# Kernel tuning notes

Hardware: AMD Instinct MI355X
Metric: run time of the kernel (lower is better)

## Reference

```python
import jax, jax.numpy as jnp
import numpy as np

D_MODEL = 1024
N_HEADS = 16
D_K = D_MODEL // N_HEADS
B, S = 4, 2048


def setup_inputs() -> dict:
    key = jax.random.key(0)
    ks = jax.random.split(key, 9)
    sc = 1.0 / np.sqrt(D_MODEL)
    return {
        "x": jax.random.normal(ks[0], (B, S, D_MODEL), dtype=jnp.float32),
        "Wq": jax.random.normal(ks[1], (D_MODEL, D_MODEL), dtype=jnp.float32) * sc,
        "bq": jax.random.normal(ks[2], (D_MODEL,), dtype=jnp.float32) * 0.02,
        "Wk": jax.random.normal(ks[3], (D_MODEL, D_MODEL), dtype=jnp.float32) * sc,
        "bk": jax.random.normal(ks[4], (D_MODEL,), dtype=jnp.float32) * 0.02,
        "Wv": jax.random.normal(ks[5], (D_MODEL, D_MODEL), dtype=jnp.float32) * sc,
        "bv": jax.random.normal(ks[6], (D_MODEL,), dtype=jnp.float32) * 0.02,
        "Wo": jax.random.normal(ks[7], (D_MODEL, D_MODEL), dtype=jnp.float32) * sc,
        "bo": jax.random.normal(ks[8], (D_MODEL,), dtype=jnp.float32) * 0.02,
    }


def reference(x, Wq, bq, Wk, bk, Wv, bv, Wo, bo):
    b, s, _ = x.shape
    # QKV projections (torch Linear: x @ W.T + b; here weights are stored as [in, out])
    q = (x @ Wq + bq).reshape(b, s, N_HEADS, D_K).transpose(0, 2, 1, 3)  # [b,h,s,dk]
    k = (x @ Wk + bk).reshape(b, s, N_HEADS, D_K).transpose(0, 2, 1, 3)
    v = (x @ Wv + bv).reshape(b, s, N_HEADS, D_K).transpose(0, 2, 1, 3)
    scores = jnp.einsum("bhqd,bhkd->bhqk", q, k) / jnp.sqrt(jnp.float32(D_K))
    attn = jax.nn.softmax(scores, axis=-1)  # dropout=0.0 -> identity
    out = jnp.einsum("bhqk,bhkd->bhqd", attn, v)
    out = out.transpose(0, 2, 1, 3).reshape(b, s, D_MODEL)
    return out @ Wo + bo
```

## Files before the change

### kernel.cpp

```cpp
#include <hip/hip_runtime.h>
#include <hip/hip_bf16.h>

#define DM    1024
#define NH    16
#define DKH   64
#define BB    4
#define SS    2048
#define MROWS (BB*SS)
#define NQKV  (3*DM)

typedef __attribute__((ext_vector_type(8))) __bf16 bf16x8;
typedef __attribute__((ext_vector_type(4))) float f32x4;
typedef __attribute__((ext_vector_type(16))) float f32x16;
typedef __attribute__((ext_vector_type(4))) unsigned short u16x4;

__device__ __forceinline__ void gload_lds16(const void* g, void* l) {
  __builtin_amdgcn_global_load_lds((const __attribute__((address_space(1))) void*)g,
                                   (__attribute__((address_space(3))) void*)l, 16, 0, 0);
}

__device__ __forceinline__ unsigned short f2bf(float f) {
  __hip_bfloat16 h = __float2bfloat16(f);
  unsigned short u;
  __builtin_memcpy(&u, &h, 2);
  return u;
}

__device__ __forceinline__ unsigned cvtpk2(float a, float b) {
  unsigned w;
  asm("v_cvt_pk_bf16_f32 %0, %1, %2" : "=v"(w) : "v"(a), "v"(b));
  return w;
}


__global__ __launch_bounds__(256) void cvt_bf16_kernel(const float* __restrict__ in,
                                                       unsigned short* __restrict__ out, int n4) {
  int i = blockIdx.x * 256 + threadIdx.x;
  if (i >= n4) return;
  float4 v = reinterpret_cast<const float4*>(in)[i];
  u16x4 o = { f2bf(v.x), f2bf(v.y), f2bf(v.z), f2bf(v.w) };
  reinterpret_cast<u16x4*>(out)[i] = o;
}

__global__ __launch_bounds__(256) void transpose_cvt4_kernel(
    const float* __restrict__ Wq, const float* __restrict__ Wk,
    const float* __restrict__ Wv, const float* __restrict__ Wo,
    unsigned short* __restrict__ WTqkv, unsigned short* __restrict__ WTo) {
  const int z = blockIdx.z;
  const float* W = (z == 0) ? Wq : (z == 1) ? Wk : (z == 2) ? Wv : Wo;
  unsigned short* WT = (z == 3) ? WTo : (WTqkv + (long)z * DM * DM);
  __shared__ float t[32][33];
  int tx = threadIdx.x & 31, ty = threadIdx.x >> 5;
  int bx = blockIdx.x * 32, by = blockIdx.y * 32;
#pragma unroll
  for (int i = 0; i < 32; i += 8)
    t[ty + i][tx] = W[(long)(by + ty + i) * DM + bx + tx];
  __syncthreads();
#pragma unroll
  for (int i = 0; i < 32; i += 8)
    WT[(long)(bx + ty + i) * DM + by + tx] = f2bf(t[tx][ty + i]);
}

__global__ void concat3_bias_kernel(const float* __restrict__ a, const float* __restrict__ b,
                                    const float* __restrict__ c, float* __restrict__ out) {
  int i = blockIdx.x * 256 + threadIdx.x;
  if (i >= NQKV) return;
  out[i] = (i < DM) ? a[i] : (i < 2 * DM) ? b[i - DM] : c[i - 2 * DM];
}


template <int MODE>
__global__ __launch_bounds__(256) void gemm_bt_kernel(
    const unsigned short* __restrict__ A,
    const unsigned short* __restrict__ BT,
    const float* __restrict__ bias,
    void* __restrict__ out0, void* __restrict__ out1, void* __restrict__ out2,
    int M, int N, int K) {
  __shared__ __align__(16) unsigned short smem[16384];
  const int tid = threadIdx.x;
  const int lane = tid & 63;
  const int lr = lane & 15, lg = lane >> 4;
  const int wv = tid >> 6, wm = wv >> 1, wn = wv & 1;
  const long bm = blockIdx.x, bn = blockIdx.y;

  const unsigned short* Ag = A + bm * 128 * K;
  const unsigned short* Bg = BT + bn * 128 * K;

  f32x4 acc[4][4];
#pragma unroll
  for (int i = 0; i < 4; ++i)
#pragma unroll
    for (int j = 0; j < 4; ++j) acc[i][j] = (f32x4){0.f, 0.f, 0.f, 0.f};

  auto issue = [&](int buf, int kt) {
#pragma unroll
    for (int it = 0; it < 2; ++it) {
      const int e = it * 2048 + tid * 8;
      const int row = e >> 5, col = e & 31;
      gload_lds16(Ag + (long)row * K + kt * 32 + col, smem + buf * 4096 + e);
      gload_lds16(Bg + (long)row * K + kt * 32 + col, smem + 8192 + buf * 4096 + e);
    }
  };

  const int NT = K / 32;
  issue(0, 0);
  issue(1, 1);
  asm volatile("s_waitcnt vmcnt(4)" ::: "memory");
  __builtin_amdgcn_s_barrier();

  for (int t = 0; t < NT; ++t) {
    const int buf = t & 1;
    const unsigned short* As_ = smem + buf * 4096;
    const unsigned short* Bs_ = smem + 8192 + buf * 4096;

    bf16x8 af[4], bfr[4];
#pragma unroll
    for (int mi = 0; mi < 4; ++mi)
      af[mi] = *reinterpret_cast<const bf16x8*>(As_ + (wm * 64 + mi * 16 + lr) * 32 + lg * 8);
#pragma unroll
    for (int ni = 0; ni < 4; ++ni)
      bfr[ni] = *reinterpret_cast<const bf16x8*>(Bs_ + (wn * 64 + ni * 16 + lr) * 32 + lg * 8);
    __builtin_amdgcn_s_setprio(1);
#pragma unroll
    for (int mi = 0; mi < 4; ++mi)
#pragma unroll
      for (int ni = 0; ni < 4; ++ni)
        acc[mi][ni] = __builtin_amdgcn_mfma_f32_16x16x32_bf16(af[mi], bfr[ni], acc[mi][ni], 0, 0, 0);
    __builtin_amdgcn_s_setprio(0);

    if (t + 1 < NT) {
      asm volatile("s_waitcnt lgkmcnt(0)" ::: "memory");
      __builtin_amdgcn_s_barrier();
      if (t + 2 < NT) {
        issue(buf, t + 2);
        asm volatile("s_waitcnt vmcnt(4)" ::: "memory");
      } else {
        asm volatile("s_waitcnt vmcnt(0)" ::: "memory");
      }
      __builtin_amdgcn_s_barrier();
      asm volatile("" ::: "memory");
    }
  }

  const float QSC = 0.125f * 1.44269504088896340736f;
#pragma unroll
  for (int ni = 0; ni < 4; ++ni) {
    const int col = (int)bn * 128 + wn * 64 + ni * 16 + lr;
    const float bc = bias[col];
#pragma unroll
    for (int mi = 0; mi < 4; ++mi) {
      const int row0 = (int)bm * 128 + wm * 64 + mi * 16 + lg * 4;
#pragma unroll
      for (int r = 0; r < 4; ++r) {
        const int row = row0 + r;
        float v = acc[mi][ni][r] + bc;
        if (MODE == 0) {
          if (col < DM) {
            ((unsigned short*)out0)[(long)row * DM + col] = f2bf(v * QSC);
          } else if (col < 2 * DM) {
            const int c2 = col - DM;
            const int h = c2 >> 6, dh = c2 & 63;
            const int b = row >> 11, s = row & 2047;
            const long idx = ((((long)(b * NH + h) * 32 + (s >> 6)) * 512 +
                               (dh >> 3) * 64 + (s & 63)) << 3) + (dh & 7);
            ((unsigned short*)out1)[idx] = f2bf(v);
          } else {
            const int c2 = col - 2 * DM;
            const int h = c2 >> 6, dh = c2 & 63;
            const int b = row >> 11, s = row & 2047;
            const long idx = ((((long)(b * NH + h) * 32 + (s >> 6)) * 512 +
                               ((s >> 3) & 7) * 64 + dh) << 3) + (s & 7);
            ((unsigned short*)out2)[idx] = f2bf(v);
          }
        } else {
          ((float*)out0)[(long)row * (long)N + col] = v;
        }
      }
    }
  }
}


__global__ __launch_bounds__(256, 3) void attn_kernel(
    const unsigned short* __restrict__ Qb,
    const unsigned short* __restrict__ Kf,
    const unsigned short* __restrict__ Vf,
    unsigned short* __restrict__ AO) {
  __shared__ __align__(16) unsigned short sK[2][4096];
  __shared__ __align__(16) unsigned short sV[2][4096];

  const int tid = threadIdx.x;
  const int lane = tid & 63;
  const int wv = tid >> 6;
  const int q5 = lane & 31;
  const int hi = lane >> 5;

  const int bh = blockIdx.x;
  const int qt = blockIdx.y;
  const int b = bh >> 4, h = bh & 15;

  bf16x8 qf[4];
  {
    const unsigned short* qrow = Qb + (long)(b * SS + qt * 128 + wv * 32 + q5) * DM + h * DKH;
#pragma unroll
    for (int dstep = 0; dstep < 4; ++dstep)
      qf[dstep] = *reinterpret_cast<const bf16x8*>(qrow + dstep * 16 + hi * 8);
  }

  const unsigned short* Kp = Kf + (long)bh * 32 * 4096;
  const unsigned short* Vp = Vf + (long)bh * 32 * 4096;

  f32x16 accv[2];
#pragma unroll
  for (int d = 0; d < 2; ++d)
#pragma unroll
    for (int r = 0; r < 16; ++r) accv[d][r] = 0.f;
  f32x16 lacc;
#pragma unroll
  for (int r = 0; r < 16; ++r) lacc[r] = 0.f;

  f32x16 zc;
#pragma unroll
  for (int r = 0; r < 16; ++r) zc[r] = 0.f;

  auto stage = [&](int buf, int t) {
#pragma unroll
    for (int it = 0; it < 2; ++it) {
      const int u = it * 256 + tid;
      gload_lds16(Kp + (long)t * 4096 + u * 8, &sK[buf][u * 8]);
      gload_lds16(Vp + (long)t * 4096 + u * 8, &sV[buf][u * 8]);
    }
  };

  stage(0, 0);
  __syncthreads();

#pragma unroll 1
  for (int kt = 0; kt < SS / 64; ++kt) {
    const int cur = kt & 1;
    if (kt + 1 < SS / 64) stage(cur ^ 1, kt + 1);
    const unsigned short* K_ = sK[cur];
    const unsigned short* V_ = sV[cur];

    f32x16 s4[2];
    __builtin_amdgcn_s_setprio(1);
#pragma unroll
    for (int kb = 0; kb < 2; ++kb)
#pragma unroll
      for (int dstep = 0; dstep < 4; ++dstep) {
        bf16x8 kf = *reinterpret_cast<const bf16x8*>(
            K_ + ((dstep * 2 + hi) * 64 + kb * 32 + q5) * 8);
        s4[kb] = __builtin_amdgcn_mfma_f32_32x32x16_bf16(kf, qf[dstep],
                                                         dstep ? s4[kb] : zc, 0, 0, 0);
      }
    __builtin_amdgcn_s_setprio(0);

#pragma unroll
    for (int kb = 0; kb < 2; ++kb)
#pragma unroll
      for (int r = 0; r < 16; ++r)
        s4[kb][r] = __builtin_amdgcn_exp2f(s4[kb][r]);
#pragma unroll
    for (int r = 0; r < 16; ++r) lacc[r] += s4[0][r] + s4[1][r];

#pragma unroll
    for (int step = 0; step < 4; ++step) {
      const int kb = step >> 1, rb = (step & 1) * 8;
      unsigned w0, w1, w2, w3;
      asm("v_cvt_pk_bf16_f32 %0, %1, %2" : "=v"(w0) : "v"(s4[kb][rb + 0]), "v"(s4[kb][rb + 1]));
      asm("v_cvt_pk_bf16_f32 %0, %1, %2" : "=v"(w1) : "v"(s4[kb][rb + 2]), "v"(s4[kb][rb + 3]));
      asm("v_cvt_pk_bf16_f32 %0, %1, %2" : "=v"(w2) : "v"(s4[kb][rb + 4]), "v"(s4[kb][rb + 5]));
      asm("v_cvt_pk_bf16_f32 %0, %1, %2" : "=v"(w3) : "v"(s4[kb][rb + 6]), "v"(s4[kb][rb + 7]));
      asm("v_permlane32_swap_b32 %0, %1" : "+v"(w0), "+v"(w2));
      asm("v_permlane32_swap_b32 %0, %1" : "+v"(w1), "+v"(w3));
      union { unsigned u[4]; bf16x8 v; } pf;
      pf.u[0] = w0;
      pf.u[1] = w1;
      pf.u[2] = w2;
      pf.u[3] = w3;
      __builtin_amdgcn_s_setprio(1);
#pragma unroll
      for (int dblk = 0; dblk < 2; ++dblk) {
        bf16x8 vf = *reinterpret_cast<const bf16x8*>(
            V_ + ((step * 2 + hi) * 64 + dblk * 32 + q5) * 8);
        accv[dblk] = __builtin_amdgcn_mfma_f32_32x32x16_bf16(vf, pf.v, accv[dblk], 0, 0, 0);
      }
      __builtin_amdgcn_s_setprio(0);
    }
    __syncthreads();
  }

  float l01 = (lacc[0] + lacc[1]) + (lacc[2] + lacc[3]);
  float l23 = (lacc[4] + lacc[5]) + (lacc[6] + lacc[7]);
  float l45 = (lacc[8] + lacc[9]) + (lacc[10] + lacc[11]);
  float l67 = (lacc[12] + lacc[13]) + (lacc[14] + lacc[15]);
  float l = (l01 + l23) + (l45 + l67);
  l += __shfl_xor(l, 32);
  const float inv = 1.0f / l;

  const long row = (long)b * SS + qt * 128 + wv * 32 + q5;
  unsigned short* orow = AO + row * DM + h * DKH;
#pragma unroll
  for (int dblk = 0; dblk < 2; ++dblk)
#pragma unroll
    for (int j = 0; j < 8; ++j) {
      const int d0 = dblk * 32 + 8 * (j >> 1) + 4 * hi + 2 * (j & 1);
      const unsigned w = cvtpk2(accv[dblk][2 * j] * inv, accv[dblk][2 * j + 1] * inv);
      *reinterpret_cast<unsigned*>(orow + d0) = w;
    }
}


extern "C" void kernel_launch(void* const* d_in, const int* in_sizes, int n_in,
                              void* d_out, int out_size, void* d_ws, size_t ws_size,
                              hipStream_t stream) {
  const float* x  = (const float*)d_in[0];
  const float* Wq = (const float*)d_in[1];
  const float* bq = (const float*)d_in[2];
  const float* Wk = (const float*)d_in[3];
  const float* bk = (const float*)d_in[4];
  const float* Wv = (const float*)d_in[5];
  const float* bv = (const float*)d_in[6];
  const float* Wo = (const float*)d_in[7];
  const float* bo = (const float*)d_in[8];
  float* out = (float*)d_out;

  char* ws = (char*)d_ws;
  size_t off = 0;
  auto alloc = [&](size_t bytes) {
    void* p = ws + off;
    off += (bytes + 255) & ~(size_t)255;
    return p;
  };
  unsigned short* Xb    = (unsigned short*)alloc((size_t)MROWS * DM * 2);
  unsigned short* WTqkv = (unsigned short*)alloc((size_t)3 * DM * DM * 2);
  unsigned short* WTo   = (unsigned short*)alloc((size_t)DM * DM * 2);
  float*          bqkv  = (float*)alloc((size_t)NQKV * 4);
  unsigned short* Qb    = (unsigned short*)alloc((size_t)MROWS * DM * 2);
  unsigned short* Kb2   = (unsigned short*)alloc((size_t)MROWS * DM * 2);
  unsigned short* Vb2   = (unsigned short*)alloc((size_t)MROWS * DM * 2);
  unsigned short* AOb   = (unsigned short*)alloc((size_t)MROWS * DM * 2);

  cvt_bf16_kernel<<<(MROWS * DM / 4 + 255) / 256, 256, 0, stream>>>(x, Xb, MROWS * DM / 4);
  transpose_cvt4_kernel<<<dim3(32, 32, 4), 256, 0, stream>>>(Wq, Wk, Wv, Wo, WTqkv, WTo);
  concat3_bias_kernel<<<(NQKV + 255) / 256, 256, 0, stream>>>(bq, bk, bv, bqkv);

  gemm_bt_kernel<0><<<dim3(MROWS / 128, NQKV / 128), 256, 0, stream>>>(
      Xb, WTqkv, bqkv, Qb, Kb2, Vb2, MROWS, NQKV, DM);

  attn_kernel<<<dim3(BB * NH, SS / 128), 256, 0, stream>>>(Qb, Kb2, Vb2, AOb);

  gemm_bt_kernel<2><<<dim3(MROWS / 128, DM / 128), 256, 0, stream>>>(
      AOb, WTo, bo, out, nullptr, nullptr, MROWS, DM, DM);
}
```

Before: 221.7 us.

## Swizzle GEMM LDS tiles and deepen attention K/V prefetch with explicit waitcnt

The GEMM's global-to-LDS staging now XOR-swizzles 16-byte column chunks by row, and the fragment reads apply the same swizzle. The goal is to cut LDS bank conflicts on the bf16x8 loads. The attention kernel now prefetches two K/V tiles ahead and uses explicit vmcnt waits with split barriers instead of a full __syncthreads per iteration, so global loads overlap compute for longer. This adds a second barrier per iteration, and it depends on the vmcnt counts matching the number of issued loads.

```diff
diff --git a/kernel.cpp b/kernel.cpp
--- a/kernel.cpp
+++ b/kernel.cpp
@@ -95,12 +95,15 @@
   auto issue = [&](int buf, int kt) {
 #pragma unroll
     for (int it = 0; it < 2; ++it) {
-      const int e = it * 2048 + tid * 8;
-      const int row = e >> 5, col = e & 31;
-      gload_lds16(Ag + (long)row * K + kt * 32 + col, smem + buf * 4096 + e);
-      gload_lds16(Bg + (long)row * K + kt * 32 + col, smem + 8192 + buf * 4096 + e);
+      const int u = it * 256 + tid;
+      const int row = u >> 2;
+      const int bL = (u & 3) ^ ((row >> 1) & 3);
+      gload_lds16(Ag + (long)row * K + kt * 32 + bL * 8, smem + buf * 4096 + u * 8);
+      gload_lds16(Bg + (long)row * K + kt * 32 + bL * 8, smem + 8192 + buf * 4096 + u * 8);
     }
   };
+
+  const int swz = (lr >> 1) & 3;
 
   const int NT = K / 32;
   issue(0, 0);
@@ -116,10 +119,12 @@
     bf16x8 af[4], bfr[4];
 #pragma unroll
     for (int mi = 0; mi < 4; ++mi)
-      af[mi] = *reinterpret_cast<const bf16x8*>(As_ + (wm * 64 + mi * 16 + lr) * 32 + lg * 8);
+      af[mi] = *reinterpret_cast<const bf16x8*>(
+          As_ + (wm * 64 + mi * 16 + lr) * 32 + ((lg ^ swz) << 3));
 #pragma unroll
     for (int ni = 0; ni < 4; ++ni)
-      bfr[ni] = *reinterpret_cast<const bf16x8*>(Bs_ + (wn * 64 + ni * 16 + lr) * 32 + lg * 8);
+      bfr[ni] = *reinterpret_cast<const bf16x8*>(
+          Bs_ + (wn * 64 + ni * 16 + lr) * 32 + ((lg ^ swz) << 3));
     __builtin_amdgcn_s_setprio(1);
 #pragma unroll
     for (int mi = 0; mi < 4; ++mi)
@@ -232,13 +237,15 @@
     }
   };
 
+  const int NT = SS / 64;
   stage(0, 0);
-  __syncthreads();
+  stage(1, 1);
+  asm volatile("s_waitcnt vmcnt(4)" ::: "memory");
+  __builtin_amdgcn_s_barrier();
 
 #pragma unroll 1
-  for (int kt = 0; kt < SS / 64; ++kt) {
+  for (int kt = 0; kt < NT; ++kt) {
     const int cur = kt & 1;
-    if (kt + 1 < SS / 64) stage(cur ^ 1, kt + 1);
     const unsigned short* K_ = sK[cur];
     const unsigned short* V_ = sV[cur];
 
@@ -287,7 +294,19 @@
       }
       __builtin_amdgcn_s_setprio(0);
     }
-    __syncthreads();
+
+    if (kt + 1 < NT) {
+      asm volatile("s_waitcnt lgkmcnt(0)" ::: "memory");
+      __builtin_amdgcn_s_barrier();
+      if (kt + 2 < NT) {
+        stage(cur, kt + 2);
+        asm volatile("s_waitcnt vmcnt(4)" ::: "memory");
+      } else {
+        asm volatile("s_waitcnt vmcnt(0)" ::: "memory");
+      }
+      __builtin_amdgcn_s_barrier();
+      asm volatile("" ::: "memory");
+    }
   }
 
   float l01 = (lacc[0] + lacc[1]) + (lacc[2] + lacc[3]);
```

Result: faster. 214.7 us (-3.1%).
